# Kernel tuning notes

Measured on AMD Instinct MI355X. Metric: run time of the kernel, lower is better.

Reference implementation:

```python
import jax, jax.numpy as jnp
import numpy as np

NUM_HEADS = 12
TOP_P = 0.9


def setup_inputs() -> dict:
    key = jax.random.key(0)
    ks = jax.random.split(key, 5)
    B, N, C = 2, 2048, 768
    return {
        "x": jax.random.normal(ks[0], (B, N, C), jnp.float32),
        "qkv_w": jax.random.normal(ks[1], (3 * C, C), jnp.float32) * (C ** -0.5),
        "proj_w": jax.random.normal(ks[2], (C, C), jnp.float32) * (C ** -0.5),
        "proj_b": jax.random.normal(ks[3], (C,), jnp.float32) * 0.02,
        "temperature": jnp.ones((1,), jnp.float32),
        "top_k": 64,
    }


def reference(x, qkv_w, proj_w, proj_b, temperature, top_k):
    B, N, C = x.shape
    H = NUM_HEADS
    D = C // H
    # qkv projection: [B,N,3C] -> [3,B,H,N,D]
    qkv = (x @ qkv_w.T).reshape(B, N, 3, H, D).transpose(2, 0, 3, 1, 4)
    q, k, v = qkv[0], qkv[1], qkv[2]
    scale = (D ** -0.5) * temperature  # (1,) broadcasts
    attn = jnp.einsum("bhnd,bhmd->bhnm", q, k) * scale  # [B,H,N,N]
    neg_inf = jnp.asarray(-jnp.inf, attn.dtype)
    # top-k filtering: keep only scores >= k-th largest per row
    kth = jax.lax.top_k(attn, top_k)[0][..., -1:]
    attn = jnp.where(attn < kth, neg_inf, attn)
    # top-p (nucleus) filtering on sorted scores
    order = jnp.argsort(-attn, axis=-1)  # descending sort indices
    sorted_attn = jnp.take_along_axis(attn, order, axis=-1)
    cum = jnp.cumsum(jax.nn.softmax(sorted_attn, axis=-1), axis=-1)
    rm = cum > TOP_P
    # shift right by one, always keep the top entry
    rm = jnp.concatenate([jnp.zeros_like(rm[..., :1]), rm[..., :-1]], axis=-1)
    # scatter back to original positions via inverse permutation
    inv = jnp.argsort(order, axis=-1)
    remove = jnp.take_along_axis(rm, inv, axis=-1)
    attn = jnp.where(remove, neg_inf, attn)
    p = jax.nn.softmax(attn, axis=-1)
    out = jnp.einsum("bhnm,bhmd->bhnd", p, v)  # [B,H,N,D]
    out = out.transpose(0, 2, 1, 3).reshape(B, N, C)
    return out @ proj_w.T + proj_b
```

## Files before the change

### kernel.cpp

```cpp
#include <hip/hip_runtime.h>
#include <cstdint>

#define NH 12
#define HD 64
#define NSEQ 2048
#define CDIM 768
#define NB 2

__global__ __launch_bounds__(256, 4) void qkv_qk(const float* __restrict__ x,
                                                 const float* __restrict__ w,
                                                 double* __restrict__ Q64,
                                                 double* __restrict__ K64,
                                                 float* __restrict__ Qs32,
                                                 float* __restrict__ Kt32) {
    __shared__ double As[16][128];
    __shared__ double Bs[16][64];
    const int tid = threadIdx.x;
    const int bm = blockIdx.y * 128;
    const int bn = blockIdx.x * 64;
    const int alm = tid >> 1, alk = (tid & 1) * 8;
    const int blm = tid & 63, blk = (tid >> 6) * 4;
    const int tx = tid & 15, ty = tid >> 4;

    double acc[8][4] = {};
    for (int k0 = 0; k0 < CDIM; k0 += 16) {
        float4 a0 = *reinterpret_cast<const float4*>(&x[(bm + alm) * CDIM + k0 + alk]);
        float4 a1 = *reinterpret_cast<const float4*>(&x[(bm + alm) * CDIM + k0 + alk + 4]);
        float4 b0 = *reinterpret_cast<const float4*>(&w[(bn + blm) * CDIM + k0 + blk]);
        __syncthreads();
        As[alk + 0][alm] = (double)a0.x; As[alk + 1][alm] = (double)a0.y;
        As[alk + 2][alm] = (double)a0.z; As[alk + 3][alm] = (double)a0.w;
        As[alk + 4][alm] = (double)a1.x; As[alk + 5][alm] = (double)a1.y;
        As[alk + 6][alm] = (double)a1.z; As[alk + 7][alm] = (double)a1.w;
        Bs[blk + 0][blm] = (double)b0.x; Bs[blk + 1][blm] = (double)b0.y;
        Bs[blk + 2][blm] = (double)b0.z; Bs[blk + 3][blm] = (double)b0.w;
        __syncthreads();
#pragma unroll
        for (int k = 0; k < 16; ++k) {
            double ad[8], bd[4];
#pragma unroll
            for (int i = 0; i < 8; ++i) ad[i] = As[k][ty * 8 + i];
#pragma unroll
            for (int j = 0; j < 4; ++j) bd[j] = Bs[k][tx * 4 + j];
#pragma unroll
            for (int i = 0; i < 8; ++i)
#pragma unroll
                for (int j = 0; j < 4; ++j) acc[i][j] = fma(ad[i], bd[j], acc[i][j]);
        }
        __syncthreads();
    }
    const bool isQ = bn < CDIM;
    const int hh = (isQ ? bn : bn - CDIM) >> 6;
    const int b  = bm >> 11;
    const int bh = b * NH + hh;
#pragma unroll
    for (int i = 0; i < 8; ++i) {
        const int n = (bm + ty * 8 + i) & (NSEQ - 1);
        const size_t base = ((size_t)bh * NSEQ + n) * HD + tx * 4;
        if (isQ) {
            double2 d01; d01.x = acc[i][0]; d01.y = acc[i][1];
            double2 d23; d23.x = acc[i][2]; d23.y = acc[i][3];
            *reinterpret_cast<double2*>(&Q64[base]) = d01;
            *reinterpret_cast<double2*>(&Q64[base + 2]) = d23;
            *reinterpret_cast<float4*>(&Qs32[base]) =
                make_float4((float)acc[i][0], (float)acc[i][1], (float)acc[i][2], (float)acc[i][3]);
        } else {
            double2 d01; d01.x = acc[i][0]; d01.y = acc[i][1];
            double2 d23; d23.x = acc[i][2]; d23.y = acc[i][3];
            *reinterpret_cast<double2*>(&K64[base]) = d01;
            *reinterpret_cast<double2*>(&K64[base + 2]) = d23;
#pragma unroll
            for (int j = 0; j < 4; ++j)
                Kt32[((size_t)bh * HD + tx * 4 + j) * NSEQ + n] = (float)acc[i][j];
        }
    }
}

__global__ __launch_bounds__(256) void qkv_v(const float* __restrict__ x,
                                             const float* __restrict__ wv,
                                             float* __restrict__ V) {
    __shared__ float As[16][64];
    __shared__ float Bs[16][64];
    const int tid = threadIdx.x;
    const int bm = blockIdx.y * 64;
    const int bn = blockIdx.x * 64;
    const int lm = tid >> 2;
    const int lk = (tid & 3) << 2;
    const int tx = tid & 15, ty = tid >> 4;

    float acc[4][4] = {};
    for (int k0 = 0; k0 < CDIM; k0 += 16) {
        float4 av = *reinterpret_cast<const float4*>(&x[(bm + lm) * CDIM + k0 + lk]);
        float4 bv = *reinterpret_cast<const float4*>(&wv[(bn + lm) * CDIM + k0 + lk]);
        __syncthreads();
        As[lk + 0][lm] = av.x; As[lk + 1][lm] = av.y; As[lk + 2][lm] = av.z; As[lk + 3][lm] = av.w;
        Bs[lk + 0][lm] = bv.x; Bs[lk + 1][lm] = bv.y; Bs[lk + 2][lm] = bv.z; Bs[lk + 3][lm] = bv.w;
        __syncthreads();
#pragma unroll
        for (int k = 0; k < 16; ++k) {
            float4 a4 = *reinterpret_cast<const float4*>(&As[k][ty * 4]);
            float4 b4 = *reinterpret_cast<const float4*>(&Bs[k][tx * 4]);
            float aa[4] = {a4.x, a4.y, a4.z, a4.w};
            float bb[4] = {b4.x, b4.y, b4.z, b4.w};
#pragma unroll
            for (int i = 0; i < 4; ++i)
#pragma unroll
                for (int j = 0; j < 4; ++j) acc[i][j] = fmaf(aa[i], bb[j], acc[i][j]);
        }
    }
    const int hh = bn >> 6;
    const int b  = bm >> 11;
#pragma unroll
    for (int i = 0; i < 4; ++i) {
        const int n = (bm + ty * 4 + i) & (NSEQ - 1);
        *reinterpret_cast<float4*>(&V[(((size_t)b * NH + hh) * NSEQ + n) * HD + tx * 4]) =
            make_float4(acc[i][0], acc[i][1], acc[i][2], acc[i][3]);
    }
}

__device__ inline unsigned long long d2key(double f) {
    unsigned long long u = (unsigned long long)__double_as_longlong(f);
    return u ^ (unsigned long long)(((long long)u >> 63) | (long long)0x8000000000000000ull);
}
__device__ inline double key2d(unsigned long long k) {
    unsigned long long mask = ((long long)k < 0) ? 0x8000000000000000ull : 0xFFFFFFFFFFFFFFFFull;
    return __longlong_as_double((long long)(k ^ mask));
}
__device__ inline unsigned kp(float a, float b) {
    unsigned ua = __float_as_uint(a);
    ua ^= (unsigned)(((int)ua >> 31) | 0x80000000);
    unsigned ub = __float_as_uint(b);
    ub ^= (unsigned)(((int)ub >> 31) | 0x80000000);
    return (ua >> 16) | (ub & 0xFFFF0000u);
}

__global__ __launch_bounds__(512, 6) void attn_kernel(const double* __restrict__ Q64,
                                                      const double* __restrict__ K64,
                                                      const float* __restrict__ Qs32,
                                                      const float* __restrict__ Kt32,
                                                      const float* __restrict__ V,
                                                      const float* __restrict__ temp,
                                                      const int* __restrict__ topk_p,
                                                      float* __restrict__ AO) {
    __shared__ unsigned short sk[8][NSEQ];
    __shared__ int cand[8][128];

    const int tid  = threadIdx.x;
    const int wg   = (blockIdx.x & 7) * 768 + (blockIdx.x >> 3);
    const int bh   = wg >> 8;
    const int g0   = (wg & 255) << 3;
    const int lane = tid & 63;
    const int wv   = tid >> 6;

    const double scale = 0.125 * (double)temp[0];
    const float sc32 = (float)scale;
    int TK = *topk_p;
    if (TK > 64) TK = 64;
    if (TK < 1)  TK = 1;

    const float* __restrict__ kb = Kt32 + (size_t)bh * HD * NSEQ;
    const float* __restrict__ qp = Qs32 + ((size_t)bh * NSEQ + g0) * HD;
    const int m0 = tid * 4;
    float acc[8][4] = {};
#pragma unroll 4
    for (int d = 0; d < HD; ++d) {
        float4 k4 = *reinterpret_cast<const float4*>(&kb[(size_t)d * NSEQ + m0]);
        float kv[4] = {k4.x, k4.y, k4.z, k4.w};
#pragma unroll
        for (int r8 = 0; r8 < 8; ++r8) {
            float qv = qp[r8 * HD + d];
#pragma unroll
            for (int c = 0; c < 4; ++c) acc[r8][c] = fmaf(qv, kv[c], acc[r8][c]);
        }
    }
#pragma unroll
    for (int r8 = 0; r8 < 8; ++r8) {
        uint2 pkv;
        pkv.x = kp(acc[r8][0] * sc32, acc[r8][1] * sc32);
        pkv.y = kp(acc[r8][2] * sc32, acc[r8][3] * sc32);
        *reinterpret_cast<uint2*>(&sk[r8][m0]) = pkv;
    }
    __syncthreads();

    const int r = wv;
    const int row = g0 + r;

    int k32[32];
#pragma unroll
    for (int i = 0; i < 32; ++i) k32[i] = sk[r][i * 64 + lane];

    int mx = k32[0];
#pragma unroll
    for (int i = 1; i < 32; ++i) mx = max(mx, k32[i]);
#pragma unroll
    for (int off = 32; off > 0; off >>= 1) mx = max(mx, __shfl_xor(mx, off));

    int lo0 = mx > 1024 ? mx - 1024 : 0;
    int c0 = 0;
#pragma unroll
    for (int i = 0; i < 32; ++i) c0 += (int)__popcll(__ballot(k32[i] >= lo0));
    int lo, hi, clo;
    if (c0 >= TK) { lo = lo0; clo = c0; hi = mx; }
    else          { lo = 0;   clo = NSEQ; hi = lo0 - 1; }
    while (lo < hi && clo > 96) {
        int mid = lo + ((hi - lo + 1) >> 1);
        int c = 0;
#pragma unroll
        for (int i = 0; i < 32; ++i) c += (int)__popcll(__ballot(k32[i] >= mid));
        if (c >= TK) { lo = mid; clo = c; } else hi = mid - 1;
    }
    int thr = lo >= 2 ? lo - 2 : 0;

    const unsigned long long lmask = (1ull << lane) - 1ull;
    int base = 0;
#pragma unroll
    for (int i = 0; i < 32; ++i) {
        bool pred = k32[i] >= thr;
        unsigned long long bal = __ballot(pred);
        if (pred) {
            int slot = base + (int)__popcll(bal & lmask);
            if (slot < 128) cand[r][slot] = i * 64 + lane;
        }
        base += (int)__popcll(bal);
    }
    int ncand = min(base, 128);
    asm volatile("s_waitcnt lgkmcnt(0)" ::: "memory");

    const int gidx = lane >> 3;
    const int sl   = lane & 7;
    const double* __restrict__ qrow = Q64 + ((size_t)bh * NSEQ + row) * HD;
    double qd[8];
#pragma unroll
    for (int j = 0; j < 8; ++j) qd[j] = qrow[sl * 8 + j];

    unsigned long long* pkr = reinterpret_cast<unsigned long long*>(&sk[r][0]);
    pkr[lane] = 0ull;
    pkr[64 + lane] = 0ull;
    const double* __restrict__ kbase = K64 + (size_t)bh * NSEQ * HD;
    const int jmax = (ncand + 7) >> 3;
    for (int j = 0; j < jmax; ++j) {
        const int s = j * 8 + gidx;
        const int ms = cand[r][min(s, ncand - 1)];
        const double* __restrict__ kp8 = kbase + (size_t)ms * HD + sl * 8;
        double a = 0.0;
#pragma unroll
        for (int d = 0; d < 8; ++d) a = fma(qd[d], kp8[d], a);
        a += __shfl_xor(a, 1);
        a += __shfl_xor(a, 2);
        a += __shfl_xor(a, 4);
        a *= scale;
        unsigned long long pkv = (d2key(a) & ~2047ull) | (unsigned long long)(2047 - ms);
        if (sl == (j & 7) && s < ncand) pkr[s] = pkv;
    }
    asm volatile("s_waitcnt lgkmcnt(0)" ::: "memory");
    unsigned long long pk1 = pkr[lane];
    unsigned long long pk2 = pkr[64 + lane];

    unsigned long long t0 = ~pk1, t1 = ~pk2;
#pragma unroll
    for (int k = 2; k <= 64; k <<= 1) {
#pragma unroll
        for (int j = k >> 1; j > 0; j >>= 1) {
            {
                unsigned long long ot = __shfl_xor(t0, j);
                bool dir = (lane & k) != 0;
                bool lower = (lane & j) == 0;
                bool takeMin = (lower != dir);
                bool less = t0 < ot;
                t0 = (takeMin == less) ? t0 : ot;
            }
            {
                unsigned long long ot = __shfl_xor(t1, j);
                bool dir = (k == 64) ? true : ((lane & k) != 0);
                bool lower = (lane & j) == 0;
                bool takeMin = (lower != dir);
                bool less = t1 < ot;
                t1 = (takeMin == less) ? t1 : ot;
            }
        }
    }
    {
        unsigned long long na = (t1 < t0) ? t1 : t0;
        unsigned long long nb = (t1 < t0) ? t0 : t1;
        t0 = na; t1 = nb;
    }
#pragma unroll
    for (int j = 32; j > 0; j >>= 1) {
        {
            unsigned long long ot = __shfl_xor(t0, j);
            bool lower = (lane & j) == 0;
            bool less = t0 < ot;
            t0 = (lower == less) ? t0 : ot;
        }
        {
            unsigned long long ot = __shfl_xor(t1, j);
            bool lower = (lane & j) == 0;
            bool less = t1 < ot;
            t1 = (lower == less) ? t1 : ot;
        }
    }
    unsigned long long kk = ~t0;
    int mi = 2047 - (int)(kk & 2047ull);
    bool valid = lane < TK;
    double a = valid ? key2d(kk & ~2047ull) : 0.0;
    double amax = __shfl(a, 0);
    double s = valid ? exp(a - amax) : 0.0;

    double ps = s;
#pragma unroll
    for (int off = 1; off < 64; off <<= 1) {
        double tt = __shfl_up(ps, off);
        if (lane >= off) ps += tt;
    }
    double S = __shfl(ps, 63);
    double cumprev = (ps - s) / S;
    bool keep = valid && ((lane == 0) || (cumprev <= 0.9));
    double sk2 = keep ? s : 0.0;
    double S2 = sk2;
#pragma unroll
    for (int off = 32; off > 0; off >>= 1) S2 += __shfl_xor(S2, off);
    float p = (float)(keep ? (s / S2) : 0.0);

    unsigned long long bal = __ballot(keep);
    int nk = __popcll(bal);

    const float* __restrict__ vb = V + (size_t)bh * NSEQ * HD;
    float o = 0.f;
    for (int i = 0; i < nk; ++i) {
        float pi = __shfl(p, i);
        int midx = __shfl(mi, i);
        o = fmaf(pi, vb[(size_t)midx * HD + lane], o);
    }
    const int b = bh / NH, hh = bh % NH;
    AO[((size_t)b * NSEQ + row) * CDIM + hh * HD + lane] = o;
}

__global__ __launch_bounds__(256) void proj_gemm(const float* __restrict__ A,
                                                 const float* __restrict__ w,
                                                 const float* __restrict__ bias,
                                                 float* __restrict__ out) {
    __shared__ float As[16][128];
    __shared__ float Bs[16][64];
    const int tid = threadIdx.x;
    const int bm = blockIdx.y * 128;
    const int bn = blockIdx.x * 64;
    const int alm = tid >> 1, alk = (tid & 1) * 8;
    const int blm = tid & 63, blk = (tid >> 6) * 4;
    const int tx = tid & 15, ty = tid >> 4;

    float acc[8][4] = {};
    for (int k0 = 0; k0 < CDIM; k0 += 16) {
        float4 a0 = *reinterpret_cast<const float4*>(&A[(bm + alm) * CDIM + k0 + alk]);
        float4 a1 = *reinterpret_cast<const float4*>(&A[(bm + alm) * CDIM + k0 + alk + 4]);
        float4 b0 = *reinterpret_cast<const float4*>(&w[(bn + blm) * CDIM + k0 + blk]);
        __syncthreads();
        As[alk + 0][alm] = a0.x; As[alk + 1][alm] = a0.y;
        As[alk + 2][alm] = a0.z; As[alk + 3][alm] = a0.w;
        As[alk + 4][alm] = a1.x; As[alk + 5][alm] = a1.y;
        As[alk + 6][alm] = a1.z; As[alk + 7][alm] = a1.w;
        Bs[blk + 0][blm] = b0.x; Bs[blk + 1][blm] = b0.y;
        Bs[blk + 2][blm] = b0.z; Bs[blk + 3][blm] = b0.w;
        __syncthreads();
#pragma unroll
        for (int k = 0; k < 16; ++k) {
            float4 af0 = *reinterpret_cast<const float4*>(&As[k][ty * 8]);
            float4 af1 = *reinterpret_cast<const float4*>(&As[k][ty * 8 + 4]);
            float4 bf  = *reinterpret_cast<const float4*>(&Bs[k][tx * 4]);
            float aa[8] = {af0.x, af0.y, af0.z, af0.w, af1.x, af1.y, af1.z, af1.w};
            float bb[4] = {bf.x, bf.y, bf.z, bf.w};
#pragma unroll
            for (int i = 0; i < 8; ++i)
#pragma unroll
                for (int j = 0; j < 4; ++j) acc[i][j] = fmaf(aa[i], bb[j], acc[i][j]);
        }
        __syncthreads();
    }
    float4 bv = *reinterpret_cast<const float4*>(&bias[bn + tx * 4]);
#pragma unroll
    for (int i = 0; i < 8; ++i) {
        int rr = bm + ty * 8 + i;
        float4 v4 = make_float4(acc[i][0] + bv.x, acc[i][1] + bv.y,
                                acc[i][2] + bv.z, acc[i][3] + bv.w);
        *reinterpret_cast<float4*>(&out[(size_t)rr * CDIM + bn + tx * 4]) = v4;
    }
}

extern "C" void kernel_launch(void* const* d_in, const int* in_sizes, int n_in,
                              void* d_out, int out_size, void* d_ws, size_t ws_size,
                              hipStream_t stream) {
    const float* x      = (const float*)d_in[0];
    const float* qkv_w  = (const float*)d_in[1];
    const float* proj_w = (const float*)d_in[2];
    const float* proj_b = (const float*)d_in[3];
    const float* temp   = (const float*)d_in[4];
    const int*   topk   = (const int*)d_in[5];
    float* out = (float*)d_out;

    const size_t HSZ = (size_t)NB * NH * NSEQ * HD;
    double* Q64  = (double*)d_ws;
    double* K64  = Q64 + HSZ;
    float*  Qs32 = (float*)(K64 + HSZ);
    float*  Kt32 = Qs32 + HSZ;
    float*  V    = Kt32 + HSZ;
    float*  AO   = V + HSZ;

    qkv_qk<<<dim3(24, 32), 256, 0, stream>>>(x, qkv_w, Q64, K64, Qs32, Kt32);
    qkv_v<<<dim3(12, 64), 256, 0, stream>>>(x, qkv_w + (size_t)2 * CDIM * CDIM, V);
    attn_kernel<<<dim3(NB * NH * (NSEQ / 8)), 512, 0, stream>>>(Q64, K64, Qs32, Kt32, V, temp, topk, AO);
    proj_gemm<<<dim3(12, 32), 256, 0, stream>>>(AO, proj_w, proj_b, out);
}
```

Before: 734.7 us.

## Prefetch GEMM tiles into registers, pack FMAs, and preload candidate indices

```diff
diff --git a/kernel.cpp b/kernel.cpp
--- a/kernel.cpp
+++ b/kernel.cpp
@@ -6,6 +6,8 @@
 #define NSEQ 2048
 #define CDIM 768
 #define NB 2
+
+typedef __attribute__((ext_vector_type(2))) float f32x2;
 
 __global__ __launch_bounds__(256, 4) void qkv_qk(const float* __restrict__ x,
                                                  const float* __restrict__ w,
@@ -23,10 +25,10 @@
     const int tx = tid & 15, ty = tid >> 4;
 
     double acc[8][4] = {};
+    float4 a0 = *reinterpret_cast<const float4*>(&x[(bm + alm) * CDIM + alk]);
+    float4 a1 = *reinterpret_cast<const float4*>(&x[(bm + alm) * CDIM + alk + 4]);
+    float4 b0 = *reinterpret_cast<const float4*>(&w[(bn + blm) * CDIM + blk]);
     for (int k0 = 0; k0 < CDIM; k0 += 16) {
-        float4 a0 = *reinterpret_cast<const float4*>(&x[(bm + alm) * CDIM + k0 + alk]);
-        float4 a1 = *reinterpret_cast<const float4*>(&x[(bm + alm) * CDIM + k0 + alk + 4]);
-        float4 b0 = *reinterpret_cast<const float4*>(&w[(bn + blm) * CDIM + k0 + blk]);
         __syncthreads();
         As[alk + 0][alm] = (double)a0.x; As[alk + 1][alm] = (double)a0.y;
         As[alk + 2][alm] = (double)a0.z; As[alk + 3][alm] = (double)a0.w;
@@ -35,6 +37,11 @@
         Bs[blk + 0][blm] = (double)b0.x; Bs[blk + 1][blm] = (double)b0.y;
         Bs[blk + 2][blm] = (double)b0.z; Bs[blk + 3][blm] = (double)b0.w;
         __syncthreads();
+        if (k0 + 16 < CDIM) {
+            a0 = *reinterpret_cast<const float4*>(&x[(bm + alm) * CDIM + k0 + 16 + alk]);
+            a1 = *reinterpret_cast<const float4*>(&x[(bm + alm) * CDIM + k0 + 16 + alk + 4]);
+            b0 = *reinterpret_cast<const float4*>(&w[(bn + blm) * CDIM + k0 + 16 + blk]);
+        }
 #pragma unroll
         for (int k = 0; k < 16; ++k) {
             double ad[8], bd[4];
@@ -47,7 +54,6 @@
 #pragma unroll
                 for (int j = 0; j < 4; ++j) acc[i][j] = fma(ad[i], bd[j], acc[i][j]);
         }
-        __syncthreads();
     }
     const bool isQ = bn < CDIM;
     const int hh = (isQ ? bn : bn - CDIM) >> 6;
@@ -89,13 +95,17 @@
     const int tx = tid & 15, ty = tid >> 4;
 
     float acc[4][4] = {};
+    float4 av = *reinterpret_cast<const float4*>(&x[(bm + lm) * CDIM + lk]);
+    float4 bv = *reinterpret_cast<const float4*>(&wv[(bn + lm) * CDIM + lk]);
     for (int k0 = 0; k0 < CDIM; k0 += 16) {
-        float4 av = *reinterpret_cast<const float4*>(&x[(bm + lm) * CDIM + k0 + lk]);
-        float4 bv = *reinterpret_cast<const float4*>(&wv[(bn + lm) * CDIM + k0 + lk]);
         __syncthreads();
         As[lk + 0][lm] = av.x; As[lk + 1][lm] = av.y; As[lk + 2][lm] = av.z; As[lk + 3][lm] = av.w;
         Bs[lk + 0][lm] = bv.x; Bs[lk + 1][lm] = bv.y; Bs[lk + 2][lm] = bv.z; Bs[lk + 3][lm] = bv.w;
         __syncthreads();
+        if (k0 + 16 < CDIM) {
+            av = *reinterpret_cast<const float4*>(&x[(bm + lm) * CDIM + k0 + 16 + lk]);
+            bv = *reinterpret_cast<const float4*>(&wv[(bn + lm) * CDIM + k0 + 16 + lk]);
+        }
 #pragma unroll
         for (int k = 0; k < 16; ++k) {
             float4 a4 = *reinterpret_cast<const float4*>(&As[k][ty * 4]);
@@ -161,23 +171,25 @@
     const float* __restrict__ kb = Kt32 + (size_t)bh * HD * NSEQ;
     const float* __restrict__ qp = Qs32 + ((size_t)bh * NSEQ + g0) * HD;
     const int m0 = tid * 4;
-    float acc[8][4] = {};
+    f32x2 acc2[8][2] = {};
 #pragma unroll 4
     for (int d = 0; d < HD; ++d) {
         float4 k4 = *reinterpret_cast<const float4*>(&kb[(size_t)d * NSEQ + m0]);
-        float kv[4] = {k4.x, k4.y, k4.z, k4.w};
+        f32x2 kA; kA.x = k4.x; kA.y = k4.y;
+        f32x2 kB; kB.x = k4.z; kB.y = k4.w;
 #pragma unroll
         for (int r8 = 0; r8 < 8; ++r8) {
             float qv = qp[r8 * HD + d];
-#pragma unroll
-            for (int c = 0; c < 4; ++c) acc[r8][c] = fmaf(qv, kv[c], acc[r8][c]);
+            f32x2 qq; qq.x = qv; qq.y = qv;
+            acc2[r8][0] = __builtin_elementwise_fma(qq, kA, acc2[r8][0]);
+            acc2[r8][1] = __builtin_elementwise_fma(qq, kB, acc2[r8][1]);
         }
     }
 #pragma unroll
     for (int r8 = 0; r8 < 8; ++r8) {
         uint2 pkv;
-        pkv.x = kp(acc[r8][0] * sc32, acc[r8][1] * sc32);
-        pkv.y = kp(acc[r8][2] * sc32, acc[r8][3] * sc32);
+        pkv.x = kp(acc2[r8][0].x * sc32, acc2[r8][0].y * sc32);
+        pkv.y = kp(acc2[r8][1].x * sc32, acc2[r8][1].y * sc32);
         *reinterpret_cast<uint2*>(&sk[r8][m0]) = pkv;
     }
     __syncthreads();
@@ -202,7 +214,7 @@
     int lo, hi, clo;
     if (c0 >= TK) { lo = lo0; clo = c0; hi = mx; }
     else          { lo = 0;   clo = NSEQ; hi = lo0 - 1; }
-    while (lo < hi && clo > 96) {
+    while (lo < hi && clo > 72) {
         int mid = lo + ((hi - lo + 1) >> 1);
         int c = 0;
 #pragma unroll
@@ -233,14 +245,19 @@
 #pragma unroll
     for (int j = 0; j < 8; ++j) qd[j] = qrow[sl * 8 + j];
 
+    int msArr[16];
+#pragma unroll
+    for (int j = 0; j < 16; ++j) msArr[j] = cand[r][min(j * 8 + gidx, ncand - 1)];
+
     unsigned long long* pkr = reinterpret_cast<unsigned long long*>(&sk[r][0]);
     pkr[lane] = 0ull;
     pkr[64 + lane] = 0ull;
     const double* __restrict__ kbase = K64 + (size_t)bh * NSEQ * HD;
     const int jmax = (ncand + 7) >> 3;
+#pragma unroll 2
     for (int j = 0; j < jmax; ++j) {
         const int s = j * 8 + gidx;
-        const int ms = cand[r][min(s, ncand - 1)];
+        const int ms = msArr[j];
         const double* __restrict__ kp8 = kbase + (size_t)ms * HD + sl * 8;
         double a = 0.0;
 #pragma unroll
@@ -349,10 +366,10 @@
     const int tx = tid & 15, ty = tid >> 4;
 
     float acc[8][4] = {};
+    float4 a0 = *reinterpret_cast<const float4*>(&A[(bm + alm) * CDIM + alk]);
+    float4 a1 = *reinterpret_cast<const float4*>(&A[(bm + alm) * CDIM + alk + 4]);
+    float4 b0 = *reinterpret_cast<const float4*>(&w[(bn + blm) * CDIM + blk]);
     for (int k0 = 0; k0 < CDIM; k0 += 16) {
-        float4 a0 = *reinterpret_cast<const float4*>(&A[(bm + alm) * CDIM + k0 + alk]);
-        float4 a1 = *reinterpret_cast<const float4*>(&A[(bm + alm) * CDIM + k0 + alk + 4]);
-        float4 b0 = *reinterpret_cast<const float4*>(&w[(bn + blm) * CDIM + k0 + blk]);
         __syncthreads();
         As[alk + 0][alm] = a0.x; As[alk + 1][alm] = a0.y;
         As[alk + 2][alm] = a0.z; As[alk + 3][alm] = a0.w;
@@ -361,6 +378,11 @@
         Bs[blk + 0][blm] = b0.x; Bs[blk + 1][blm] = b0.y;
         Bs[blk + 2][blm] = b0.z; Bs[blk + 3][blm] = b0.w;
         __syncthreads();
+        if (k0 + 16 < CDIM) {
+            a0 = *reinterpret_cast<const float4*>(&A[(bm + alm) * CDIM + k0 + 16 + alk]);
+            a1 = *reinterpret_cast<const float4*>(&A[(bm + alm) * CDIM + k0 + 16 + alk + 4]);
+            b0 = *reinterpret_cast<const float4*>(&w[(bn + blm) * CDIM + k0 + 16 + blk]);
+        }
 #pragma unroll
         for (int k = 0; k < 16; ++k) {
             float4 af0 = *reinterpret_cast<const float4*>(&As[k][ty * 8]);
@@ -373,7 +395,6 @@
 #pragma unroll
                 for (int j = 0; j < 4; ++j) acc[i][j] = fmaf(aa[i], bb[j], acc[i][j]);
         }
-        __syncthreads();
     }
     float4 bv = *reinterpret_cast<const float4*>(&bias[bn + tx * 4]);
 #pragma unroll
```

Measured after the change: 715.5 us. 1.03x faster.
